# Kernel optimization log

Hardware: AMD Instinct MI355X
Metric: run time of the kernel (lower is better)

The kernel has to match this reference:

```python
import jax, jax.numpy as jnp
import numpy as np

HIDDEN, DOWN, UP, NH, RHD = 2048, 512, 1024, 16, 64
HEAD_DIM = HIDDEN // NH        # 128 (used only in the score scale)
V_HEAD = UP // NH              # 64
BASE = 10000.0


def _rope(q):
    # q: [bs, heads, seq, d] with even d. Faithful to the torch module,
    # including its swapped sin/cos cache names.
    d = q.shape[-1]
    seq = q.shape[2]
    theta = BASE ** (-jnp.arange(0, d, 2, dtype=jnp.float32) / d)      # [d/2]
    pos = jnp.arange(seq, dtype=jnp.float32)[:, None] * theta[None, :]  # [seq, d/2]
    cos_pos = jnp.repeat(jnp.sin(pos), 2, axis=-1)  # torch code: cos_pos = sin(...)
    sin_pos = jnp.repeat(jnp.cos(pos), 2, axis=-1)  # torch code: sin_pos = cos(...)
    q2 = jnp.stack([-q[..., 1::2], q[..., ::2]], axis=-1).reshape(q.shape)
    return q * cos_pos[None, None] + q2 * sin_pos[None, None]


def setup_inputs() -> dict:
    key = jax.random.key(0)
    ks = jax.random.split(key, 12)
    bs, seq = 16, 512

    def lin(k, fan_in, fan_out):
        kw, kb = jax.random.split(k)
        bound = 1.0 / np.sqrt(fan_in)
        W = jax.random.uniform(kw, (fan_in, fan_out), jnp.float32, -bound, bound)
        b = jax.random.uniform(kb, (fan_out,), jnp.float32, -bound, bound)
        return W, b

    x = jax.random.normal(ks[0], (bs, seq, HIDDEN), jnp.float32)
    mask = jax.random.randint(ks[1], (bs, seq), 0, 2, jnp.int32)
    w_dkv, b_dkv = lin(ks[2], HIDDEN, DOWN)
    w_dq, b_dq = lin(ks[3], HIDDEN, DOWN)
    w_uq, b_uq = lin(ks[4], DOWN, UP)
    w_uk, b_uk = lin(ks[5], DOWN, UP)
    w_uv, b_uv = lin(ks[6], DOWN, UP)
    w_qr, b_qr = lin(ks[7], DOWN, RHD * NH)
    w_kr, b_kr = lin(ks[8], DOWN, RHD)
    w_fc, b_fc = lin(ks[9], NH * V_HEAD, HIDDEN)
    return dict(x=x, mask=mask, w_dkv=w_dkv, b_dkv=b_dkv, w_dq=w_dq, b_dq=b_dq,
                w_uq=w_uq, b_uq=b_uq, w_uk=w_uk, b_uk=b_uk, w_uv=w_uv, b_uv=b_uv,
                w_qr=w_qr, b_qr=b_qr, w_kr=w_kr, b_kr=b_kr, w_fc=w_fc, b_fc=b_fc)


def reference(x, mask, w_dkv, b_dkv, w_dq, b_dq, w_uq, b_uq, w_uk, b_uk,
              w_uv, b_uv, w_qr, b_qr, w_kr, b_kr, w_fc, b_fc):
    bs, seq, _ = x.shape
    # latent down-projections
    c_kv = x @ w_dkv + b_dkv                       # [bs, seq, DOWN]
    c_q = x @ w_dq + b_dq                          # [bs, seq, DOWN]
    # content up-projections
    k_c = (c_kv @ w_uk + b_uk).reshape(bs, seq, NH, UP // NH).transpose(0, 2, 1, 3)
    v_c = (c_kv @ w_uv + b_uv).reshape(bs, seq, NH, V_HEAD).transpose(0, 2, 1, 3)
    q_c = (c_q @ w_uq + b_uq).reshape(bs, seq, NH, UP // NH).transpose(0, 2, 1, 3)
    # rope branches
    q_r = (c_q @ w_qr + b_qr).reshape(bs, seq, NH, RHD).transpose(0, 2, 1, 3)
    q_r = _rope(q_r)                               # [bs, NH, seq, RHD]
    k_r = (c_kv @ w_kr + b_kr)[:, None]            # [bs, 1, seq, RHD]
    k_r = _rope(k_r)
    # concat content + rope dims
    q = jnp.concatenate([q_c, q_r], axis=-1)                        # [bs,NH,seq,UP/NH+RHD]
    k = jnp.concatenate([k_c, jnp.broadcast_to(k_r, (bs, NH, seq, RHD))], axis=-1)
    scale = 1.0 / (HEAD_DIM ** 0.5 + RHD ** 0.5)
    scores = jnp.einsum('bhqd,bhkd->bhqk', q, k) * scale
    scores = jnp.where(mask[:, None, None, :] == 0, -jnp.inf, scores)
    attn = jax.nn.softmax(scores, axis=-1)
    ctx = jnp.einsum('bhqk,bhkd->bhqd', attn, v_c)                  # [bs,NH,seq,V_HEAD]
    ctx = ctx.transpose(0, 2, 1, 3).reshape(bs, seq, NH * V_HEAD)
    return ctx @ w_fc + b_fc
```

## Files before the change

### kernel.cpp

```cpp
#include <hip/hip_runtime.h>
#include <cstdint>
#include <cmath>

typedef unsigned short u16;
typedef unsigned int   u32;
typedef _Float16 f16x8 __attribute__((ext_vector_type(8)));
typedef float f32x4  __attribute__((ext_vector_type(4)));

#define MFMAH(a, b, c) __builtin_amdgcn_mfma_f32_16x16x32_f16((a), (b), (c), 0, 0, 0)

__device__ __forceinline__ u16 f2h(float f) {
  _Float16 h = (_Float16)f;
  return __builtin_bit_cast(u16, h);
}
__device__ __forceinline__ float h2f(u16 u) {
  return (float)__builtin_bit_cast(_Float16, u);
}
__device__ __forceinline__ float fexp2(float x) { return __builtin_amdgcn_exp2f(x); }
__device__ __forceinline__ void async16(const void* g, void* l) {
  __builtin_amdgcn_global_load_lds((const __attribute__((address_space(1))) u32*)g,
                                   (__attribute__((address_space(3))) u32*)l, 16, 0, 0);
}

__global__ void convert_x_kernel(const float* __restrict__ x, u16* __restrict__ xh, int n4) {
  int i = blockIdx.x * blockDim.x + threadIdx.x;
  if (i >= n4) return;
  float4 v = reinterpret_cast<const float4*>(x)[i];
  uint2 p;
  p.x = (u32)f2h(v.x) | ((u32)f2h(v.y) << 16);
  p.y = (u32)f2h(v.z) | ((u32)f2h(v.w) << 16);
  reinterpret_cast<uint2*>(xh)[i] = p;
}

template <int NOUT>
__global__ void wtrans_kernel(const float* __restrict__ W, int N,
                              u16* __restrict__ Thi, u16* __restrict__ Tlo,
                              int row_off, int dst_ld) {
  __shared__ float tile[32][33];
  int k0 = blockIdx.x * 32, n0 = blockIdx.y * 32;
  int tx = threadIdx.x & 31, ty = threadIdx.x >> 5;
#pragma unroll
  for (int i = 0; i < 32; i += 8)
    tile[ty + i][tx] = W[(size_t)(k0 + ty + i) * N + n0 + tx];
  __syncthreads();
#pragma unroll
  for (int i = 0; i < 32; i += 8) {
    float v = tile[tx][ty + i];
    size_t o = (size_t)(row_off + n0 + ty + i) * dst_ld + k0 + tx;
    u16 h = f2h(v);
    Thi[o] = h;
    if constexpr (NOUT == 2) Tlo[o] = f2h(v - h2f(h));
  }
}

template <int MODE, int TERMS>
__global__ __launch_bounds__(256, TERMS == 2 ? 3 : 4) void gemmh_kernel(
    const u16* __restrict__ Ah, int lda,
    const u16* __restrict__ Bhi, const u16* __restrict__ Blo, int ldb,
    const float* __restrict__ bias, const float* __restrict__ bias2, int bsplit,
    void* __restrict__ out0, int N, int K, int ldc) {
  __shared__ u16 lA[128 * 64];
  __shared__ u16 lB[TERMS][128 * 64];
  const int tid = threadIdx.x;
  const int wave = tid >> 6, lane = tid & 63;
  const int lrow = lane & 15, kgrp = lane >> 4;
  const int nwg = gridDim.x * gridDim.y;
  const int orig = blockIdx.y * gridDim.x + blockIdx.x;
  const int swz = (orig & 7) * (nwg >> 3) + (orig >> 3);
  const int bm = (swz % gridDim.x) * 128, bn = (swz / gridDim.x) * 128;
  const int wm = (wave >> 1) * 64, wn = (wave & 1) * 64;
  const int srow = lane >> 3, sg = lane & 7;

  f32x4 acc[4][4];
  const f32x4 zero = {0.f, 0.f, 0.f, 0.f};
#pragma unroll
  for (int i = 0; i < 4; ++i)
#pragma unroll
    for (int j = 0; j < 4; ++j) acc[i][j] = zero;

  for (int kt = 0; kt < K; kt += 64) {
#pragma unroll
    for (int ii = 0; ii < 4; ++ii) {
      int inst = wave * 4 + ii;
      int row = inst * 8 + srow;
      int koff = kt + ((sg ^ (row & 7)) << 3);
      async16(Ah + (size_t)(bm + row) * lda + koff, &lA[inst * 512]);
      int brow = bn + row;
      if (brow > N - 1) brow = N - 1;
      async16(Bhi + (size_t)brow * ldb + koff, &lB[0][inst * 512]);
      if constexpr (TERMS == 2)
        async16(Blo + (size_t)brow * ldb + koff, &lB[TERMS - 1][inst * 512]);
    }
    asm volatile("s_waitcnt vmcnt(0)" ::: "memory");
    __syncthreads();

#pragma unroll
    for (int ks = 0; ks < 2; ++ks) {
      f16x8 ah[4], b0v[4], b1v[4];
#pragma unroll
      for (int mi = 0; mi < 4; ++mi) {
        int row = wm + mi * 16 + lrow;
        int off = row * 128 + ((ks * 64 + kgrp * 16) ^ ((row & 7) << 4));
        ah[mi] = *(const f16x8*)((const char*)lA + off);
      }
#pragma unroll
      for (int ni = 0; ni < 4; ++ni) {
        int row = wn + ni * 16 + lrow;
        int off = row * 128 + ((ks * 64 + kgrp * 16) ^ ((row & 7) << 4));
        b0v[ni] = *(const f16x8*)((const char*)lB[0] + off);
        if constexpr (TERMS == 2)
          b1v[ni] = *(const f16x8*)((const char*)lB[TERMS - 1] + off);
      }
#pragma unroll
      for (int mi = 0; mi < 4; ++mi)
#pragma unroll
        for (int ni = 0; ni < 4; ++ni) {
          acc[mi][ni] = MFMAH(ah[mi], b0v[ni], acc[mi][ni]);
          if constexpr (TERMS == 2)
            acc[mi][ni] = MFMAH(ah[mi], b1v[ni], acc[mi][ni]);
        }
    }
    __syncthreads();
  }

#pragma unroll
  for (int mi = 0; mi < 4; ++mi) {
#pragma unroll
    for (int ni = 0; ni < 4; ++ni) {
      int col = bn + wn + ni * 16 + lrow;
      if (col >= N) continue;
      float bv = (col < bsplit) ? bias[col] : bias2[col - bsplit];
      int row0 = bm + wm + mi * 16 + kgrp * 4;
#pragma unroll
      for (int r = 0; r < 4; ++r) {
        int row = row0 + r;
        float v = acc[mi][ni][r] + bv;
        if (MODE == 0) {
          ((float*)out0)[(size_t)row * ldc + col] = v;
        } else if (MODE == 3) {
          ((u16*)out0)[(size_t)row * ldc + col] = f2h(v);
        } else {
          int bb = row >> 9, ss = row & 511, hh = col >> 6, dd = col & 63;
          ((u16*)out0)[(((size_t)(bb * 16 + hh) * 512 + ss) << 7) + dd] = f2h(v);
        }
      }
    }
  }
}

__global__ void ropeq_kernel(const float* __restrict__ qr, u16* __restrict__ Qb) {
  int idx = blockIdx.x * 256 + threadIdx.x;
  int t = idx >> 9;
  int rem = idx & 511;
  int h = rem >> 5, i = rem & 31;
  float2 v = reinterpret_cast<const float2*>(qr + (size_t)t * 1024 + h * 64)[i];
  float theta = exp2f((float)i * (-13.287712379549449f / 32.0f));
  float ang = (float)(t & 511) * theta;
  float sn = sinf(ang), cs = cosf(ang);
  float o0 = v.x * sn - v.y * cs;
  float o1 = v.y * sn + v.x * cs;
  size_t o = ((size_t)((t >> 9) * 16 + h) * 512 + (t & 511)) * 128 + 64 + 2 * i;
  u32 pk = (u32)f2h(o0) | ((u32)f2h(o1) << 16);
  *reinterpret_cast<u32*>(Qb + o) = pk;
}

__global__ void ropek_kernel(const float* __restrict__ kr, u16* __restrict__ Kb) {
  int idx = blockIdx.x * 256 + threadIdx.x;
  int t = idx >> 5, i = idx & 31;
  float2 v = reinterpret_cast<const float2*>(kr + (size_t)t * 64)[i];
  float theta = exp2f((float)i * (-13.287712379549449f / 32.0f));
  float ang = (float)(t & 511) * theta;
  float sn = sinf(ang), cs = cosf(ang);
  float o0 = v.x * sn - v.y * cs;
  float o1 = v.y * sn + v.x * cs;
  u32 pk = (u32)f2h(o0) | ((u32)f2h(o1) << 16);
  int bb = t >> 9, ss = t & 511;
  size_t base = (size_t)bb * 16 * 512 * 128;
#pragma unroll
  for (int hh = 0; hh < 16; ++hh)
    *reinterpret_cast<u32*>(Kb + base + ((size_t)(hh * 512 + ss)) * 128 + 64 + 2 * i) = pk;
}

__global__ void vtrans_kernel(const float* __restrict__ v, u16* __restrict__ Vt) {
  __shared__ u16 tl[64][65];
  const int bh = blockIdx.x, b = bh >> 4, h = bh & 15;
  const int s0 = blockIdx.y * 64;
  const int tid = threadIdx.x;
  const int d = tid & 63, si = tid >> 6;
#pragma unroll
  for (int i = 0; i < 64; i += 4)
    tl[si + i][d] = f2h(v[((size_t)(b * 512 + s0 + si + i)) * 1024 + h * 64 + d]);
  __syncthreads();
  const int sj = tid & 63, dd = tid >> 6;
#pragma unroll
  for (int i = 0; i < 64; i += 4)
    Vt[((size_t)bh * 64 + dd + i) * 512 + s0 + sj] = tl[sj][dd + i];
}

__global__ __launch_bounds__(256, 3) void attn_kernel(
    const u16* __restrict__ Qb, const u16* __restrict__ Kb, const u16* __restrict__ Vt,
    const int* __restrict__ mask, u16* __restrict__ ctx,
    float scale2) {
  __shared__ u16 sQ[64 * 128];
  __shared__ u16 sK[64 * 128];
  __shared__ u16 sV[64 * 64];
  __shared__ u16 sP[4][16 * 64];
  const int tid = threadIdx.x, wave = tid >> 6, lane = tid & 63;
  const int lrow = lane & 15, kgrp = lane >> 4;
  const int bh = blockIdx.x, b = bh >> 4, h = bh & 15;
  const int q0 = blockIdx.y * 64;
  const size_t qkbase = (size_t)bh * 512 * 128;
  const size_t vbase = (size_t)bh * 64 * 512;
  u16* __restrict__ sPw = sP[wave];

  u32 poff[4][4];
#pragma unroll
  for (int r = 0; r < 4; ++r) {
    int qp = kgrp * 4 + r;
    int xr = (qp & 7) << 3;
#pragma unroll
    for (int nf = 0; nf < 4; ++nf) poff[r][nf] = (u32)((qp * 64 + nf * 16 + lrow) ^ xr);
  }

  {
    int g = lane & 15, rr = lane >> 4;
#pragma unroll
    for (int ii = 0; ii < 4; ++ii) {
      int inst = wave * 4 + ii;
      int row = inst * 4 + rr;
      int perm = (g & 8) | ((g & 7) ^ (row & 7));
      async16(Qb + qkbase + (size_t)(q0 + row) * 128 + perm * 8, &sQ[inst * 512]);
    }
  }

  const f32x4 zero = {0.f, 0.f, 0.f, 0.f};
  f32x4 O[4];
#pragma unroll
  for (int nf = 0; nf < 4; ++nf) O[nf] = zero;
  float m_run[4], l_run[4];
#pragma unroll
  for (int r = 0; r < 4; ++r) { m_run[r] = -1e30f; l_run[r] = 0.f; }

  for (int kvt = 0; kvt < 8; ++kvt) {
    const int kv0 = kvt * 64;
    {
      int g = lane & 15, rr = lane >> 4;
#pragma unroll
      for (int ii = 0; ii < 4; ++ii) {
        int inst = wave * 4 + ii;
        int row = inst * 4 + rr;
        int perm = (g & 8) | ((g & 7) ^ (row & 7));
        async16(Kb + qkbase + (size_t)(kv0 + row) * 128 + perm * 8, &sK[inst * 512]);
      }
      int g2 = lane & 7, r2 = lane >> 3;
#pragma unroll
      for (int ii = 0; ii < 2; ++ii) {
        int inst = wave * 2 + ii;
        int row = inst * 8 + r2;
        async16(Vt + vbase + (size_t)row * 512 + kv0 + ((g2 ^ (row & 7)) << 3),
                &sV[inst * 512]);
      }
    }
    float mb[4];
#pragma unroll
    for (int nf = 0; nf < 4; ++nf)
      mb[nf] = (mask[b * 512 + kv0 + nf * 16 + lrow] != 0) ? 0.f : -1e30f;

    asm volatile("s_waitcnt vmcnt(0)" ::: "memory");
    __syncthreads();

    f32x4 S[4];
#pragma unroll
    for (int nf = 0; nf < 4; ++nf) S[nf] = zero;
#pragma unroll
    for (int ks = 0; ks < 4; ++ks) {
      int qrow = wave * 16 + lrow;
      int kb = ks * 64 + kgrp * 16;
      f16x8 aq = *(const f16x8*)((const char*)sQ + qrow * 256 + (kb ^ ((qrow & 7) << 4)));
#pragma unroll
      for (int nf = 0; nf < 4; ++nf) {
        int krow = nf * 16 + lrow;
        f16x8 bk = *(const f16x8*)((const char*)sK + krow * 256 + (kb ^ ((krow & 7) << 4)));
        S[nf] = MFMAH(aq, bk, S[nf]);
      }
    }

    float pvv[4][4];
    float tmax[4] = {-1e30f, -1e30f, -1e30f, -1e30f};
#pragma unroll
    for (int nf = 0; nf < 4; ++nf) {
#pragma unroll
      for (int r = 0; r < 4; ++r) {
        float v = fmaf(S[nf][r], scale2, mb[nf]);
        pvv[nf][r] = v;
        tmax[r] = fmaxf(tmax[r], v);
      }
    }
#pragma unroll
    for (int r = 0; r < 4; ++r) {
#pragma unroll
      for (int mv = 1; mv < 16; mv <<= 1)
        tmax[r] = fmaxf(tmax[r], __shfl_xor(tmax[r], mv, 64));
    }
#pragma unroll
    for (int r = 0; r < 4; ++r) {
      float newm = fmaxf(m_run[r], tmax[r]);
      float sc = fexp2(m_run[r] - newm);
      m_run[r] = newm;
      float ts = 0.f;
#pragma unroll
      for (int nf = 0; nf < 4; ++nf) {
        float pe = fexp2(pvv[nf][r] - newm);
        sPw[poff[r][nf]] = f2h(pe);
        ts += pe;
      }
#pragma unroll
      for (int mv = 1; mv < 16; mv <<= 1) ts += __shfl_xor(ts, mv, 64);
      l_run[r] = l_run[r] * sc + ts;
#pragma unroll
      for (int nf = 0; nf < 4; ++nf) O[nf][r] *= sc;
    }

#pragma unroll
    for (int ks = 0; ks < 2; ++ks) {
      int kb = ks * 64 + kgrp * 16;
      f16x8 ap = *(const f16x8*)((const char*)sPw + ((lrow * 128 + kb) ^ ((lrow & 7) << 4)));
#pragma unroll
      for (int nf = 0; nf < 4; ++nf) {
        int vr = nf * 16 + lrow;
        f16x8 bv = *(const f16x8*)((const char*)sV + vr * 128 + (kb ^ ((vr & 7) << 4)));
        O[nf] = MFMAH(ap, bv, O[nf]);
      }
    }
    __syncthreads();
  }

#pragma unroll
  for (int r = 0; r < 4; ++r) {
    float inv = 1.0f / l_run[r];
    int trow = b * 512 + q0 + wave * 16 + kgrp * 4 + r;
#pragma unroll
    for (int nf = 0; nf < 4; ++nf) {
      int col = h * 64 + nf * 16 + lrow;
      ctx[(size_t)trow * 1024 + col] = f2h(O[nf][r] * inv);
    }
  }
}

extern "C" void kernel_launch(void* const* d_in, const int* in_sizes, int n_in,
                              void* d_out, int out_size, void* d_ws, size_t ws_size,
                              hipStream_t stream) {
  const float* x     = (const float*)d_in[0];
  const int*   mask  = (const int*)d_in[1];
  const float* w_dkv = (const float*)d_in[2];
  const float* b_dkv = (const float*)d_in[3];
  const float* w_dq  = (const float*)d_in[4];
  const float* b_dq  = (const float*)d_in[5];
  const float* w_uq  = (const float*)d_in[6];
  const float* b_uq  = (const float*)d_in[7];
  const float* w_uk  = (const float*)d_in[8];
  const float* b_uk  = (const float*)d_in[9];
  const float* w_uv  = (const float*)d_in[10];
  const float* b_uv  = (const float*)d_in[11];
  const float* w_qr  = (const float*)d_in[12];
  const float* b_qr  = (const float*)d_in[13];
  const float* w_kr  = (const float*)d_in[14];
  const float* b_kr  = (const float*)d_in[15];
  const float* w_fc  = (const float*)d_in[16];
  const float* b_fc  = (const float*)d_in[17];
  float* out = (float*)d_out;

  char* ws = (char*)d_ws;
  size_t off = 0;
  auto alloc = [&](size_t bytes) -> void* {
    void* p = ws + off;
    off += (bytes + 255) & ~(size_t)255;
    return p;
  };
  u16* xh    = (u16*)alloc(33554432);
  u16* WfTh  = (u16*)alloc(4194304);
  u16* WfTl  = (u16*)alloc(4194304);
  u16* WuqT  = (u16*)alloc(1048576);
  u16* WqrT  = (u16*)alloc(1048576);
  u16* WukT  = (u16*)alloc(1048576);
  u16* WuvT  = (u16*)alloc(1048576);
  u16* WkrT  = (u16*)alloc(65536);
  u16* WfcTh = (u16*)alloc(4194304);
  u16* WfcTl = (u16*)alloc(4194304);
  u16* c     = (u16*)alloc(16777216);
  u16* Qb    = (u16*)alloc(33554432);
  u16* Kb    = (u16*)alloc(33554432);
  u16* Vt    = (u16*)alloc(16777216);
  float* krf = (float*)alloc(2097152);
  float* vf  = (float*)alloc(33554432);
  float* qrf = (float*)xh;
  u16* ctx  = c;
  (void)ws_size; (void)in_sizes; (void)n_in; (void)out_size;

  const float scale = 1.0f / (sqrtf(128.0f) + sqrtf(64.0f));
  const float scale2 = scale * 1.4426950408889634f;

  convert_x_kernel<<<16384, 256, 0, stream>>>(x, xh, 4194304);
  wtrans_kernel<2><<<dim3(64, 16), 256, 0, stream>>>(w_dkv, 512, WfTh, WfTl, 0, 2048);
  wtrans_kernel<2><<<dim3(64, 16), 256, 0, stream>>>(w_dq, 512, WfTh, WfTl, 512, 2048);
  wtrans_kernel<1><<<dim3(16, 32), 256, 0, stream>>>(w_uq, 1024, WuqT, nullptr, 0, 512);
  wtrans_kernel<1><<<dim3(16, 32), 256, 0, stream>>>(w_qr, 1024, WqrT, nullptr, 0, 512);
  wtrans_kernel<1><<<dim3(16, 32), 256, 0, stream>>>(w_uk, 1024, WukT, nullptr, 0, 512);
  wtrans_kernel<1><<<dim3(16, 32), 256, 0, stream>>>(w_uv, 1024, WuvT, nullptr, 0, 512);
  wtrans_kernel<1><<<dim3(16, 2), 256, 0, stream>>>(w_kr, 64, WkrT, nullptr, 0, 512);
  wtrans_kernel<2><<<dim3(32, 64), 256, 0, stream>>>(w_fc, 2048, WfcTh, WfcTl, 0, 1024);

  gemmh_kernel<3, 2><<<dim3(64, 8), 256, 0, stream>>>(
      xh, 2048, WfTh, WfTl, 2048, b_dkv, b_dq, 512,
      (void*)c, 1024, 2048, 1024);
  gemmh_kernel<2, 1><<<dim3(64, 8), 256, 0, stream>>>(
      c + 512, 1024, WuqT, nullptr, 512, b_uq, b_uq, 1024,
      (void*)Qb, 1024, 512, 0);
  gemmh_kernel<0, 1><<<dim3(64, 8), 256, 0, stream>>>(
      c + 512, 1024, WqrT, nullptr, 512, b_qr, b_qr, 1024,
      (void*)qrf, 1024, 512, 1024);
  gemmh_kernel<2, 1><<<dim3(64, 8), 256, 0, stream>>>(
      c, 1024, WukT, nullptr, 512, b_uk, b_uk, 1024,
      (void*)Kb, 1024, 512, 0);
  gemmh_kernel<0, 1><<<dim3(64, 8), 256, 0, stream>>>(
      c, 1024, WuvT, nullptr, 512, b_uv, b_uv, 1024,
      (void*)vf, 1024, 512, 1024);
  gemmh_kernel<0, 1><<<dim3(64, 1), 256, 0, stream>>>(
      c, 1024, WkrT, nullptr, 512, b_kr, b_kr, 64,
      (void*)krf, 64, 512, 64);

  ropeq_kernel<<<16384, 256, 0, stream>>>(qrf, Qb);
  ropek_kernel<<<1024, 256, 0, stream>>>(krf, Kb);
  vtrans_kernel<<<dim3(256, 8), 256, 0, stream>>>(vf, Vt);

  attn_kernel<<<dim3(256, 8), 256, 0, stream>>>(Qb, Kb, Vt, mask, ctx, scale2);

  gemmh_kernel<0, 2><<<dim3(64, 16), 256, 0, stream>>>(
      ctx, 1024, WfcTh, WfcTl, 1024, b_fc, b_fc, 2048,
      (void*)out, 2048, 1024, 2048);
}
```

Before: 500.7 us.

## Fuse up-projection GEMMs with RoPE/V-transpose epilogues and add lazy softmax rescale

Concatenates the Q-side weights (uq+qr) and KV-side weights (uk+uv+kr) so each side runs as one GEMM launch. RoPE for q and the V transpose now happen in the GEMM epilogue, which removes the ropeq and vtrans kernels and their fp32 intermediate round-trips. RoPE sin/cos values come from a precomputed table. In attention, the online softmax now rescales only when the max grows by more than a threshold, defers the row-sum reduction to the end, and changes the P layout in LDS. The risks are a larger epilogue with shuffles and branches, and padded bias/weight tiles for the N=2176 case.

```diff
diff --git a/kernel.cpp b/kernel.cpp
--- a/kernel.cpp
+++ b/kernel.cpp
@@ -20,6 +20,27 @@
 __device__ __forceinline__ void async16(const void* g, void* l) {
   __builtin_amdgcn_global_load_lds((const __attribute__((address_space(1))) u32*)g,
                                    (__attribute__((address_space(3))) u32*)l, 16, 0, 0);
+}
+
+__global__ void stab_kernel(float2* __restrict__ stab) {
+  int idx = blockIdx.x * 256 + threadIdx.x;
+  int s = idx >> 5, i = idx & 31;
+  float theta = exp2f((float)i * (-13.287712379549449f / 32.0f));
+  float ang = (float)s * theta;
+  stab[idx] = make_float2(sinf(ang), cosf(ang));
+}
+
+__global__ void biascat_kernel(const float* __restrict__ buq, const float* __restrict__ bqr,
+                               const float* __restrict__ buk, const float* __restrict__ buv,
+                               const float* __restrict__ bkr,
+                               float* __restrict__ biasQ, float* __restrict__ biasKV) {
+  int idx = blockIdx.x * 256 + threadIdx.x;
+  if (idx < 2048) biasQ[idx] = (idx < 1024) ? buq[idx] : bqr[idx - 1024];
+  int j = idx - 2048;
+  if (j >= 0 && j < 2176)
+    biasKV[j] = (j < 1024) ? buk[j]
+              : (j < 2048) ? buv[j - 1024]
+              : (j < 2112) ? bkr[j - 2048] : 0.f;
 }
 
 __global__ void convert_x_kernel(const float* __restrict__ x, u16* __restrict__ xh, int n4) {
@@ -58,7 +79,8 @@
     const u16* __restrict__ Ah, int lda,
     const u16* __restrict__ Bhi, const u16* __restrict__ Blo, int ldb,
     const float* __restrict__ bias, const float* __restrict__ bias2, int bsplit,
-    void* __restrict__ out0, int N, int K, int ldc) {
+    void* __restrict__ out0, void* __restrict__ out1, void* __restrict__ out2,
+    const float2* __restrict__ stab, int N, int K, int ldc) {
   __shared__ u16 lA[128 * 64];
   __shared__ u16 lB[TERMS][128 * 64];
   const int tid = threadIdx.x;
@@ -128,73 +150,80 @@
 #pragma unroll
     for (int ni = 0; ni < 4; ++ni) {
       int col = bn + wn + ni * 16 + lrow;
-      if (col >= N) continue;
       float bv = (col < bsplit) ? bias[col] : bias2[col - bsplit];
       int row0 = bm + wm + mi * 16 + kgrp * 4;
-#pragma unroll
-      for (int r = 0; r < 4; ++r) {
-        int row = row0 + r;
-        float v = acc[mi][ni][r] + bv;
-        if (MODE == 0) {
-          ((float*)out0)[(size_t)row * ldc + col] = v;
-        } else if (MODE == 3) {
-          ((u16*)out0)[(size_t)row * ldc + col] = f2h(v);
+      if constexpr (MODE == 0) {
+#pragma unroll
+        for (int r = 0; r < 4; ++r)
+          ((float*)out0)[(size_t)(row0 + r) * ldc + col] = acc[mi][ni][r] + bv;
+      } else if constexpr (MODE == 3) {
+#pragma unroll
+        for (int r = 0; r < 4; ++r)
+          ((u16*)out0)[(size_t)(row0 + r) * ldc + col] = f2h(acc[mi][ni][r] + bv);
+      } else if constexpr (MODE == 7) {
+        if (col < 1024) {
+#pragma unroll
+          for (int r = 0; r < 4; ++r) {
+            int row = row0 + r;
+            ((u16*)out0)[(((size_t)((row >> 9) * 16 + (col >> 6)) * 512 + (row & 511)) << 7)
+                         + (col & 63)] = f2h(acc[mi][ni][r] + bv);
+          }
         } else {
-          int bb = row >> 9, ss = row & 511, hh = col >> 6, dd = col & 63;
-          ((u16*)out0)[(((size_t)(bb * 16 + hh) * 512 + ss) << 7) + dd] = f2h(v);
+          int cc = col - 1024, hh = cc >> 6, d = cc & 63, i2 = d >> 1;
+          bool odd = d & 1;
+#pragma unroll
+          for (int r = 0; r < 4; ++r) {
+            int row = row0 + r, s = row & 511;
+            float vv = acc[mi][ni][r] + bv;
+            float p = __shfl_xor(vv, 1, 64);
+            float2 t2 = stab[s * 32 + i2];
+            float o = odd ? (vv * t2.x + p * t2.y) : (vv * t2.x - p * t2.y);
+            ((u16*)out0)[(((size_t)((row >> 9) * 16 + hh) * 512 + (row & 511)) << 7)
+                         + 64 + d] = f2h(o);
+          }
         }
-      }
-    }
-  }
-}
-
-__global__ void ropeq_kernel(const float* __restrict__ qr, u16* __restrict__ Qb) {
-  int idx = blockIdx.x * 256 + threadIdx.x;
-  int t = idx >> 9;
-  int rem = idx & 511;
-  int h = rem >> 5, i = rem & 31;
-  float2 v = reinterpret_cast<const float2*>(qr + (size_t)t * 1024 + h * 64)[i];
-  float theta = exp2f((float)i * (-13.287712379549449f / 32.0f));
-  float ang = (float)(t & 511) * theta;
-  float sn = sinf(ang), cs = cosf(ang);
-  float o0 = v.x * sn - v.y * cs;
-  float o1 = v.y * sn + v.x * cs;
-  size_t o = ((size_t)((t >> 9) * 16 + h) * 512 + (t & 511)) * 128 + 64 + 2 * i;
-  u32 pk = (u32)f2h(o0) | ((u32)f2h(o1) << 16);
-  *reinterpret_cast<u32*>(Qb + o) = pk;
-}
-
-__global__ void ropek_kernel(const float* __restrict__ kr, u16* __restrict__ Kb) {
+      } else if constexpr (MODE == 6) {
+        if (col < 1024) {
+#pragma unroll
+          for (int r = 0; r < 4; ++r) {
+            int row = row0 + r;
+            ((u16*)out0)[(((size_t)((row >> 9) * 16 + (col >> 6)) * 512 + (row & 511)) << 7)
+                         + (col & 63)] = f2h(acc[mi][ni][r] + bv);
+          }
+        } else if (col < 2048) {
+          int cc = col - 1024;
+          u16 h0 = f2h(acc[mi][ni][0] + bv), h1 = f2h(acc[mi][ni][1] + bv);
+          u16 h2 = f2h(acc[mi][ni][2] + bv), h3 = f2h(acc[mi][ni][3] + bv);
+          uint2 pk;
+          pk.x = (u32)h0 | ((u32)h1 << 16);
+          pk.y = (u32)h2 | ((u32)h3 << 16);
+          size_t base = ((size_t)((row0 >> 9) * 16 + (cc >> 6)) * 64 + (cc & 63)) * 512
+                        + (row0 & 511);
+          *reinterpret_cast<uint2*>((u16*)out1 + base) = pk;
+        } else {
+#pragma unroll
+          for (int r = 0; r < 4; ++r)
+            ((float*)out2)[(size_t)(row0 + r) * 128 + (col - 2048)] = acc[mi][ni][r] + bv;
+        }
+      }
+    }
+  }
+}
+
+__global__ void ropek_kernel(const float* __restrict__ kr, const float2* __restrict__ stab,
+                             u16* __restrict__ Kb) {
   int idx = blockIdx.x * 256 + threadIdx.x;
   int t = idx >> 5, i = idx & 31;
-  float2 v = reinterpret_cast<const float2*>(kr + (size_t)t * 64)[i];
-  float theta = exp2f((float)i * (-13.287712379549449f / 32.0f));
-  float ang = (float)(t & 511) * theta;
-  float sn = sinf(ang), cs = cosf(ang);
-  float o0 = v.x * sn - v.y * cs;
-  float o1 = v.y * sn + v.x * cs;
+  float vx = kr[(size_t)t * 128 + 2 * i], vy = kr[(size_t)t * 128 + 2 * i + 1];
+  float2 t2 = stab[(t & 511) * 32 + i];
+  float o0 = vx * t2.x - vy * t2.y;
+  float o1 = vy * t2.x + vx * t2.y;
   u32 pk = (u32)f2h(o0) | ((u32)f2h(o1) << 16);
   int bb = t >> 9, ss = t & 511;
   size_t base = (size_t)bb * 16 * 512 * 128;
 #pragma unroll
   for (int hh = 0; hh < 16; ++hh)
     *reinterpret_cast<u32*>(Kb + base + ((size_t)(hh * 512 + ss)) * 128 + 64 + 2 * i) = pk;
-}
-
-__global__ void vtrans_kernel(const float* __restrict__ v, u16* __restrict__ Vt) {
-  __shared__ u16 tl[64][65];
-  const int bh = blockIdx.x, b = bh >> 4, h = bh & 15;
-  const int s0 = blockIdx.y * 64;
-  const int tid = threadIdx.x;
-  const int d = tid & 63, si = tid >> 6;
-#pragma unroll
-  for (int i = 0; i < 64; i += 4)
-    tl[si + i][d] = f2h(v[((size_t)(b * 512 + s0 + si + i)) * 1024 + h * 64 + d]);
-  __syncthreads();
-  const int sj = tid & 63, dd = tid >> 6;
-#pragma unroll
-  for (int i = 0; i < 64; i += 4)
-    Vt[((size_t)bh * 64 + dd + i) * 512 + s0 + sj] = tl[sj][dd + i];
 }
 
 __global__ __launch_bounds__(256, 3) void attn_kernel(
@@ -204,7 +233,7 @@
   __shared__ u16 sQ[64 * 128];
   __shared__ u16 sK[64 * 128];
   __shared__ u16 sV[64 * 64];
-  __shared__ u16 sP[4][16 * 64];
+  __shared__ u16 sP[4][1024];
   const int tid = threadIdx.x, wave = tid >> 6, lane = tid & 63;
   const int lrow = lane & 15, kgrp = lane >> 4;
   const int bh = blockIdx.x, b = bh >> 4, h = bh & 15;
@@ -217,9 +246,10 @@
 #pragma unroll
   for (int r = 0; r < 4; ++r) {
     int qp = kgrp * 4 + r;
-    int xr = (qp & 7) << 3;
-#pragma unroll
-    for (int nf = 0; nf < 4; ++nf) poff[r][nf] = (u32)((qp * 64 + nf * 16 + lrow) ^ xr);
+#pragma unroll
+    for (int nf = 0; nf < 4; ++nf)
+      poff[r][nf] = (u32)((nf >> 1) * 512 + ((((nf & 1) << 1) | (lrow >> 3))) * 128
+                          + qp * 8 + (lrow & 7));
   }
 
   {
@@ -237,9 +267,9 @@
   f32x4 O[4];
 #pragma unroll
   for (int nf = 0; nf < 4; ++nf) O[nf] = zero;
-  float m_run[4], l_run[4];
-#pragma unroll
-  for (int r = 0; r < 4; ++r) { m_run[r] = -1e30f; l_run[r] = 0.f; }
+  float m_run[4], l_part[4];
+#pragma unroll
+  for (int r = 0; r < 4; ++r) { m_run[r] = -1e30f; l_part[r] = 0.f; }
 
   for (int kvt = 0; kvt < 8; ++kvt) {
     const int kv0 = kvt * 64;
@@ -286,7 +316,9 @@
     }
 
     float pvv[4][4];
-    float tmax[4] = {-1e30f, -1e30f, -1e30f, -1e30f};
+    float tmax[4];
+#pragma unroll
+    for (int r = 0; r < 4; ++r) tmax[r] = -1e30f;
 #pragma unroll
     for (int nf = 0; nf < 4; ++nf) {
 #pragma unroll
@@ -302,29 +334,44 @@
       for (int mv = 1; mv < 16; mv <<= 1)
         tmax[r] = fmaxf(tmax[r], __shfl_xor(tmax[r], mv, 64));
     }
-#pragma unroll
-    for (int r = 0; r < 4; ++r) {
-      float newm = fmaxf(m_run[r], tmax[r]);
-      float sc = fexp2(m_run[r] - newm);
-      m_run[r] = newm;
-      float ts = 0.f;
-#pragma unroll
-      for (int nf = 0; nf < 4; ++nf) {
-        float pe = fexp2(pvv[nf][r] - newm);
-        sPw[poff[r][nf]] = f2h(pe);
-        ts += pe;
-      }
-#pragma unroll
-      for (int mv = 1; mv < 16; mv <<= 1) ts += __shfl_xor(ts, mv, 64);
-      l_run[r] = l_run[r] * sc + ts;
-#pragma unroll
-      for (int nf = 0; nf < 4; ++nf) O[nf][r] *= sc;
+
+    bool grow = (tmax[0] > m_run[0] + 8.f) || (tmax[1] > m_run[1] + 8.f) ||
+                (tmax[2] > m_run[2] + 8.f) || (tmax[3] > m_run[3] + 8.f);
+    if (__any(grow ? 1 : 0)) {
+#pragma unroll
+      for (int r = 0; r < 4; ++r) {
+        float newm = fmaxf(m_run[r], tmax[r]);
+        float sc = fexp2(m_run[r] - newm);
+        m_run[r] = newm;
+        float ts = 0.f;
+#pragma unroll
+        for (int nf = 0; nf < 4; ++nf) {
+          float pe = fexp2(pvv[nf][r] - newm);
+          sPw[poff[r][nf]] = f2h(pe);
+          ts += pe;
+        }
+        l_part[r] = l_part[r] * sc + ts;
+#pragma unroll
+        for (int nf = 0; nf < 4; ++nf) O[nf][r] *= sc;
+      }
+    } else {
+#pragma unroll
+      for (int r = 0; r < 4; ++r) {
+        float ts = 0.f;
+#pragma unroll
+        for (int nf = 0; nf < 4; ++nf) {
+          float pe = fexp2(pvv[nf][r] - m_run[r]);
+          sPw[poff[r][nf]] = f2h(pe);
+          ts += pe;
+        }
+        l_part[r] += ts;
+      }
     }
 
 #pragma unroll
     for (int ks = 0; ks < 2; ++ks) {
       int kb = ks * 64 + kgrp * 16;
-      f16x8 ap = *(const f16x8*)((const char*)sPw + ((lrow * 128 + kb) ^ ((lrow & 7) << 4)));
+      f16x8 ap = *(const f16x8*)((const char*)sPw + ((ks * 64 + kgrp * 16 + lrow) << 4));
 #pragma unroll
       for (int nf = 0; nf < 4; ++nf) {
         int vr = nf * 16 + lrow;
@@ -337,7 +384,13 @@
 
 #pragma unroll
   for (int r = 0; r < 4; ++r) {
-    float inv = 1.0f / l_run[r];
+#pragma unroll
+    for (int mv = 1; mv < 16; mv <<= 1) l_part[r] += __shfl_xor(l_part[r], mv, 64);
+  }
+
+#pragma unroll
+  for (int r = 0; r < 4; ++r) {
+    float inv = 1.0f / l_part[r];
     int trow = b * 512 + q0 + wave * 16 + kgrp * 4 + r;
 #pragma unroll
     for (int nf = 0; nf < 4; ++nf) {
@@ -377,65 +430,54 @@
     off += (bytes + 255) & ~(size_t)255;
     return p;
   };
-  u16* xh    = (u16*)alloc(33554432);
-  u16* WfTh  = (u16*)alloc(4194304);
-  u16* WfTl  = (u16*)alloc(4194304);
-  u16* WuqT  = (u16*)alloc(1048576);
-  u16* WqrT  = (u16*)alloc(1048576);
-  u16* WukT  = (u16*)alloc(1048576);
-  u16* WuvT  = (u16*)alloc(1048576);
-  u16* WkrT  = (u16*)alloc(65536);
-  u16* WfcTh = (u16*)alloc(4194304);
-  u16* WfcTl = (u16*)alloc(4194304);
-  u16* c     = (u16*)alloc(16777216);
-  u16* Qb    = (u16*)alloc(33554432);
-  u16* Kb    = (u16*)alloc(33554432);
-  u16* Vt    = (u16*)alloc(16777216);
-  float* krf = (float*)alloc(2097152);
-  float* vf  = (float*)alloc(33554432);
-  float* qrf = (float*)xh;
-  u16* ctx  = c;
+  u16* xh     = (u16*)alloc(33554432);
+  u16* WfTh   = (u16*)alloc(4194304);
+  u16* WfTl   = (u16*)alloc(4194304);
+  u16* WqT    = (u16*)alloc(2097152);
+  u16* WkvT   = (u16*)alloc(2228224);
+  u16* WfcTh  = (u16*)alloc(4194304);
+  u16* WfcTl  = (u16*)alloc(4194304);
+  u16* c      = (u16*)alloc(16777216);
+  u16* Qb     = (u16*)alloc(33554432);
+  u16* Kb     = (u16*)alloc(33554432);
+  u16* Vt     = (u16*)alloc(16777216);
+  float* krf  = (float*)alloc(4194304);
+  float2* stab = (float2*)alloc(131072);
+  float* biasQ  = (float*)alloc(8192);
+  float* biasKV = (float*)alloc(8704);
+  u16* ctx = c;
   (void)ws_size; (void)in_sizes; (void)n_in; (void)out_size;
 
   const float scale = 1.0f / (sqrtf(128.0f) + sqrtf(64.0f));
   const float scale2 = scale * 1.4426950408889634f;
 
+  stab_kernel<<<64, 256, 0, stream>>>(stab);
   convert_x_kernel<<<16384, 256, 0, stream>>>(x, xh, 4194304);
+  biascat_kernel<<<17, 256, 0, stream>>>(b_uq, b_qr, b_uk, b_uv, b_kr, biasQ, biasKV);
   wtrans_kernel<2><<<dim3(64, 16), 256, 0, stream>>>(w_dkv, 512, WfTh, WfTl, 0, 2048);
   wtrans_kernel<2><<<dim3(64, 16), 256, 0, stream>>>(w_dq, 512, WfTh, WfTl, 512, 2048);
-  wtrans_kernel<1><<<dim3(16, 32), 256, 0, stream>>>(w_uq, 1024, WuqT, nullptr, 0, 512);
-  wtrans_kernel<1><<<dim3(16, 32), 256, 0, stream>>>(w_qr, 1024, WqrT, nullptr, 0, 512);
-  wtrans_kernel<1><<<dim3(16, 32), 256, 0, stream>>>(w_uk, 1024, WukT, nullptr, 0, 512);
-  wtrans_kernel<1><<<dim3(16, 32), 256, 0, stream>>>(w_uv, 1024, WuvT, nullptr, 0, 512);
-  wtrans_kernel<1><<<dim3(16, 2), 256, 0, stream>>>(w_kr, 64, WkrT, nullptr, 0, 512);
+  wtrans_kernel<1><<<dim3(16, 32), 256, 0, stream>>>(w_uq, 1024, WqT, nullptr, 0, 512);
+  wtrans_kernel<1><<<dim3(16, 32), 256, 0, stream>>>(w_qr, 1024, WqT, nullptr, 1024, 512);
+  wtrans_kernel<1><<<dim3(16, 32), 256, 0, stream>>>(w_uk, 1024, WkvT, nullptr, 0, 512);
+  wtrans_kernel<1><<<dim3(16, 32), 256, 0, stream>>>(w_uv, 1024, WkvT, nullptr, 1024, 512);
+  wtrans_kernel<1><<<dim3(16, 2), 256, 0, stream>>>(w_kr, 64, WkvT, nullptr, 2048, 512);
   wtrans_kernel<2><<<dim3(32, 64), 256, 0, stream>>>(w_fc, 2048, WfcTh, WfcTl, 0, 1024);
 
   gemmh_kernel<3, 2><<<dim3(64, 8), 256, 0, stream>>>(
       xh, 2048, WfTh, WfTl, 2048, b_dkv, b_dq, 512,
-      (void*)c, 1024, 2048, 1024);
-  gemmh_kernel<2, 1><<<dim3(64, 8), 256, 0, stream>>>(
-      c + 512, 1024, WuqT, nullptr, 512, b_uq, b_uq, 1024,
-      (void*)Qb, 1024, 512, 0);
-  gemmh_kernel<0, 1><<<dim3(64, 8), 256, 0, stream>>>(
-      c + 512, 1024, WqrT, nullptr, 512, b_qr, b_qr, 1024,
-      (void*)qrf, 1024, 512, 1024);
-  gemmh_kernel<2, 1><<<dim3(64, 8), 256, 0, stream>>>(
-      c, 1024, WukT, nullptr, 512, b_uk, b_uk, 1024,
-      (void*)Kb, 1024, 512, 0);
-  gemmh_kernel<0, 1><<<dim3(64, 8), 256, 0, stream>>>(
-      c, 1024, WuvT, nullptr, 512, b_uv, b_uv, 1024,
-      (void*)vf, 1024, 512, 1024);
-  gemmh_kernel<0, 1><<<dim3(64, 1), 256, 0, stream>>>(
-      c, 1024, WkrT, nullptr, 512, b_kr, b_kr, 64,
-      (void*)krf, 64, 512, 64);
-
-  ropeq_kernel<<<16384, 256, 0, stream>>>(qrf, Qb);
-  ropek_kernel<<<1024, 256, 0, stream>>>(krf, Kb);
-  vtrans_kernel<<<dim3(256, 8), 256, 0, stream>>>(vf, Vt);
+      (void*)c, nullptr, nullptr, nullptr, 1024, 2048, 1024);
+  gemmh_kernel<7, 1><<<dim3(64, 16), 256, 0, stream>>>(
+      c + 512, 1024, WqT, nullptr, 512, biasQ, biasQ, 2048,
+      (void*)Qb, nullptr, nullptr, stab, 2048, 512, 0);
+  gemmh_kernel<6, 1><<<dim3(64, 17), 256, 0, stream>>>(
+      c, 1024, WkvT, nullptr, 512, biasKV, biasKV, 2176,
+      (void*)Kb, (void*)Vt, (void*)krf, nullptr, 2176, 512, 0);
+
+  ropek_kernel<<<1024, 256, 0, stream>>>(krf, stab, Kb);
 
   attn_kernel<<<dim3(256, 8), 256, 0, stream>>>(Qb, Kb, Vt, mask, ctx, scale2);
 
   gemmh_kernel<0, 2><<<dim3(64, 16), 256, 0, stream>>>(
       ctx, 1024, WfcTh, WfcTl, 1024, b_fc, b_fc, 2048,
-      (void*)out, 2048, 1024, 2048);
-}
+      (void*)out, nullptr, nullptr, nullptr, 2048, 1024, 2048);
+}
```

After: 458.7 us. 8.4% less time.
